# Performance work log

Hardware: AMD Instinct MI355X
Metric: run time of the kernel (lower is better)

Reference implementation:

```python
import jax, jax.numpy as jnp
import numpy as np
from math import sqrt

EMBED_DIM = 1024
PROJ_DIM = 128
BATCH = 4
SEQ = 4096


def setup_inputs() -> dict:
    key = jax.random.key(0)
    ks = jax.random.split(key, 7)
    x = jax.random.normal(ks[0], (BATCH, SEQ, EMBED_DIM), dtype=jnp.float32)
    # nn.Linear default init scale ~ 1/sqrt(fan_in); use small random weights
    s_e = 1.0 / sqrt(EMBED_DIM)
    Wq = jax.random.uniform(ks[1], (EMBED_DIM, PROJ_DIM), jnp.float32, -s_e, s_e)
    bq = jax.random.uniform(ks[2], (PROJ_DIM,), jnp.float32, -s_e, s_e)
    Wk = jax.random.uniform(ks[3], (EMBED_DIM, PROJ_DIM), jnp.float32, -s_e, s_e)
    bk = jax.random.uniform(ks[4], (PROJ_DIM,), jnp.float32, -s_e, s_e)
    Wov = jax.random.uniform(ks[5], (EMBED_DIM, EMBED_DIM), jnp.float32, -s_e, s_e)
    bov = jax.random.uniform(ks[6], (EMBED_DIM,), jnp.float32, -s_e, s_e)
    return {"x": x, "Wq": Wq, "bq": bq, "Wk": Wk, "bk": bk, "Wov": Wov, "bov": bov}


def reference(x, Wq, bq, Wk, bk, Wov, bov):
    # q, k: (b, s, p); ov: (b, s, d)
    queries = jnp.einsum('bse,ep->bsp', x, Wq) + bq
    keys = jnp.einsum('bse,ep->bsp', x, Wk) + bk
    scores = jnp.einsum('bqp,bkp->bqk', queries, keys) / sqrt(PROJ_DIM)
    pattern = jax.nn.softmax(scores, axis=-1)
    ov = jnp.einsum('bse,ed->bsd', x, Wov) + bov
    return jnp.einsum('bqk,bkd->bqd', pattern, ov)
```

## Files before the change

### kernel.cpp

```cpp
#include <hip/hip_runtime.h>
#include <hip/hip_bf16.h>

#define BATCH 4
#define SEQ   4096
#define EMB   1024
#define PDIM  128

using short8   = __attribute__((ext_vector_type(8))) short;
using ushort8  = __attribute__((ext_vector_type(8))) unsigned short;
using ushort4v = __attribute__((ext_vector_type(4))) unsigned short;
using float4v  = __attribute__((ext_vector_type(4))) float;
using float16v = __attribute__((ext_vector_type(16))) float;

__device__ __forceinline__ unsigned short f2bf(float f) {
  union { float f; unsigned int u; } x; x.f = f;
  unsigned int r = x.u + 0x7fffu + ((x.u >> 16) & 1u);
  return (unsigned short)(r >> 16);
}

__device__ __forceinline__ void gld_lds16(const unsigned short* g, unsigned short* l) {
  __builtin_amdgcn_global_load_lds(
      (__attribute__((address_space(1))) void*)(g),
      (__attribute__((address_space(3))) void*)(l), 16, 0, 0);
}

__global__ void xprep_kernel(const float* __restrict__ src,
                             unsigned short* __restrict__ rm,
                             unsigned short* __restrict__ tp) {
  __shared__ float tile[64][65];
  const int tid = threadIdx.x;
  const int z = blockIdx.z;
  const float* s = src + (size_t)z * SEQ * EMB;
  unsigned short* drm = rm + (size_t)z * SEQ * EMB;
  unsigned short* dtp = tp + (size_t)z * SEQ * EMB;
  const int e0 = blockIdx.x * 64, s0 = blockIdx.y * 64;
#pragma unroll
  for (int i = 0; i < 4; i++) {
    int idx = tid + i * 256;
    int sr = idx >> 4, c4 = (idx & 15) * 4;
    float4v v = *(const float4v*)(s + (size_t)(s0 + sr) * EMB + e0 + c4);
    ushort4v o;
    o[0] = f2bf(v[0]); o[1] = f2bf(v[1]); o[2] = f2bf(v[2]); o[3] = f2bf(v[3]);
    *(ushort4v*)(drm + (size_t)(s0 + sr) * EMB + e0 + c4) = o;
    tile[sr][c4] = v[0]; tile[sr][c4 + 1] = v[1];
    tile[sr][c4 + 2] = v[2]; tile[sr][c4 + 3] = v[3];
  }
  __syncthreads();
#pragma unroll
  for (int i = 0; i < 2; i++) {
    int idx = tid + i * 256;
    int e = idx >> 3, sc = idx & 7;
    ushort8 o;
#pragma unroll
    for (int j = 0; j < 8; j++) o[j] = f2bf(tile[sc * 8 + j][e]);
    *(ushort8*)(dtp + (size_t)(e0 + e) * SEQ + s0 + sc * 8) = o;
  }
}

__global__ void wprep_kernel(const float* __restrict__ Wq, const float* __restrict__ Wk,
                             const float* __restrict__ Wov,
                             unsigned short* __restrict__ WqkT, unsigned short* __restrict__ WovT,
                             const float* __restrict__ bq, const float* __restrict__ bk,
                             float* __restrict__ bqk, float* __restrict__ lsum) {
  __shared__ float t[32][33];
  const int bid = blockIdx.x, tid = threadIdx.x;
  const int tx = tid & 31, ty = tid >> 5;
  const float* src; unsigned short* dst; int C, bx, by;
  if (bid < 128)        { src = Wq;  dst = WqkT;                       C = PDIM; int b = bid;        bx = b & 3;  by = b >> 2; }
  else if (bid < 256)   { src = Wk;  dst = WqkT + (size_t)PDIM * EMB;  C = PDIM; int b = bid - 128;  bx = b & 3;  by = b >> 2; }
  else if (bid < 1280)  { src = Wov; dst = WovT;                       C = EMB;  int b = bid - 256;  bx = b & 31; by = b >> 5; }
  else if (bid == 1280) {
    if (tid < 2 * PDIM) bqk[tid] = (tid < PDIM) ? bq[tid] : bk[tid - PDIM];
    return;
  } else {
    lsum[(bid - 1281) * 256 + tid] = 0.f;
    return;
  }
  const int c0 = bx * 32, r0 = by * 32;
#pragma unroll
  for (int i = 0; i < 32; i += 8)
    t[ty + i][tx] = src[(size_t)(r0 + ty + i) * C + c0 + tx];
  __syncthreads();
#pragma unroll
  for (int i = 0; i < 32; i += 8)
    dst[(size_t)(c0 + ty + i) * EMB + r0 + tx] = f2bf(t[tx][ty + i]);
}

template <int NT>
__global__ __launch_bounds__(256, 2) void gemm_kernel(
    const unsigned short* __restrict__ A, int lda, size_t saz,
    const unsigned short* __restrict__ Bt, int ldb, size_t sbz,
    void* __restrict__ Cv, int ldc, size_t scz,
    int K, const float* __restrict__ bias,
    float* __restrict__ lsum, int slz,
    float scale, int mode) {
  constexpr int NTW = NT / 64;
  constexpr int BC  = NT / 32;
  __shared__ __attribute__((aligned(16))) unsigned short As[128 * 64];
  __shared__ __attribute__((aligned(16))) unsigned short Bs[NT * 64];
  const int tid = threadIdx.x;
  const int wave = tid >> 6, lane = tid & 63;
  const int m0 = blockIdx.x * 128, n0 = blockIdx.y * NT;
  const int z = blockIdx.z;
  const int mq = (wave >> 1) * 64, nq = (wave & 1) * (NT / 2);

  A  += (size_t)z * saz;
  Bt += (size_t)z * sbz;

  const int sr = lane >> 3, sc = lane & 7;
  const int kch = (sc ^ sr) * 8;
  const unsigned short* Ag[4]; unsigned short* Al[4];
#pragma unroll
  for (int j = 0; j < 4; j++) {
    int c = wave * 4 + j;
    Ag[j] = A + (size_t)(m0 + c * 8 + sr) * lda + kch;
    Al[j] = As + c * 512;
  }
  const unsigned short* Bg[BC]; unsigned short* Bl[BC];
#pragma unroll
  for (int j = 0; j < BC; j++) {
    int c = wave * BC + j;
    Bg[j] = Bt + (size_t)(n0 + c * 8 + sr) * ldb + kch;
    Bl[j] = Bs + c * 512;
  }

  float16v acc[2][NTW];
#pragma unroll
  for (int i = 0; i < 2; i++)
#pragma unroll
    for (int j = 0; j < NTW; j++)
#pragma unroll
      for (int r = 0; r < 16; r++) acc[i][j][r] = 0.f;

  const int rt = lane & 31;
  const int h  = lane >> 5;
  const int s7 = lane & 7;

  for (int k0 = 0; k0 < K; k0 += 64) {
    if (k0) __syncthreads();
#pragma unroll
    for (int j = 0; j < 4; j++) gld_lds16(Ag[j] + k0, Al[j]);
#pragma unroll
    for (int j = 0; j < BC; j++) gld_lds16(Bg[j] + k0, Bl[j]);
    __syncthreads();
#pragma unroll
    for (int kt = 0; kt < 4; kt++) {
      const int sl = ((kt * 2 + h) ^ s7) * 8;
      short8 af[2], bfr[NTW];
#pragma unroll
      for (int mt = 0; mt < 2; mt++)
        af[mt] = *(const short8*)(As + (mq + mt * 32 + rt) * 64 + sl);
#pragma unroll
      for (int nt = 0; nt < NTW; nt++)
        bfr[nt] = *(const short8*)(Bs + (nq + nt * 32 + rt) * 64 + sl);
#pragma unroll
      for (int mt = 0; mt < 2; mt++)
#pragma unroll
        for (int nt = 0; nt < NTW; nt++)
          acc[mt][nt] = __builtin_amdgcn_mfma_f32_32x32x16_bf16(af[mt], bfr[nt], acc[mt][nt], 0, 0, 0);
    }
  }

  if (mode == 1) {
    unsigned short* Cb = (unsigned short*)Cv + (size_t)z * scz;
    float* ls = lsum + (size_t)z * slz;
#pragma unroll
    for (int mt = 0; mt < 2; mt++) {
      float rs[16];
#pragma unroll
      for (int r = 0; r < 16; r++) rs[r] = 0.f;
#pragma unroll
      for (int r = 0; r < 16; r++) {
        int gm = m0 + mq + mt * 32 + (r & 3) + 8 * (r >> 2) + 4 * h;
#pragma unroll
        for (int nt = 0; nt < NTW; nt++) {
          float e = __expf(acc[mt][nt][r] * scale);
          Cb[(size_t)gm * ldc + n0 + nq + nt * 32 + rt] = f2bf(e);
          rs[r] += e;
        }
      }
#pragma unroll
      for (int r = 0; r < 16; r++) {
        float s = rs[r];
#pragma unroll
        for (int o = 1; o < 32; o <<= 1) s += __shfl_xor(s, o);
        rs[r] = s;
      }
      if (rt == 0)
#pragma unroll
        for (int r = 0; r < 16; r++)
          atomicAdd(&ls[m0 + mq + mt * 32 + (r & 3) + 8 * (r >> 2) + 4 * h], rs[r]);
    }
  } else if (mode == 2) {
    unsigned short* Cb = (unsigned short*)Cv + (size_t)z * scz;
    const float* ls = lsum + (size_t)z * slz;
#pragma unroll
    for (int mt = 0; mt < 2; mt++)
#pragma unroll
      for (int r = 0; r < 16; r++) {
        int gm = m0 + mq + mt * 32 + (r & 3) + 8 * (r >> 2) + 4 * h;
        float li = 1.f / ls[gm];
#pragma unroll
        for (int nt = 0; nt < NTW; nt++)
          Cb[(size_t)gm * ldc + n0 + nq + nt * 32 + rt] = f2bf(acc[mt][nt][r] * li);
      }
  } else {
    float* Cf = (float*)Cv + (size_t)z * scz;
    unsigned short* Cb = (unsigned short*)Cv + (size_t)z * scz;
    float bv[NTW];
#pragma unroll
    for (int nt = 0; nt < NTW; nt++) bv[nt] = bias[n0 + nq + nt * 32 + rt];
#pragma unroll
    for (int mt = 0; mt < 2; mt++)
#pragma unroll
      for (int r = 0; r < 16; r++) {
        int gm = m0 + mq + mt * 32 + (r & 3) + 8 * (r >> 2) + 4 * h;
#pragma unroll
        for (int nt = 0; nt < NTW; nt++) {
          float v = acc[mt][nt][r] + bv[nt];
          if (mode == 0) Cf[(size_t)gm * ldc + n0 + nq + nt * 32 + rt] = v;
          else           Cb[(size_t)gm * ldc + n0 + nq + nt * 32 + rt] = f2bf(v);
        }
      }
  }
}

extern "C" void kernel_launch(void* const* d_in, const int* in_sizes, int n_in,
                              void* d_out, int out_size, void* d_ws, size_t ws_size,
                              hipStream_t stream) {
  const float* x   = (const float*)d_in[0];
  const float* Wq  = (const float*)d_in[1];
  const float* bq  = (const float*)d_in[2];
  const float* Wk  = (const float*)d_in[3];
  const float* bk  = (const float*)d_in[4];
  const float* Wov = (const float*)d_in[5];
  const float* bov = (const float*)d_in[6];
  float* out = (float*)d_out;

  char* ws = (char*)d_ws;
  size_t off = 0;
  auto alloc = [&](size_t bytes) {
    char* p = ws + off;
    off += (bytes + 255) & ~(size_t)255;
    return p;
  };
  const int M = BATCH * SEQ;
  unsigned short* x_bf = (unsigned short*)alloc((size_t)M * EMB * 2);
  unsigned short* xT   = (unsigned short*)alloc((size_t)M * EMB * 2);
  unsigned short* WqkT = (unsigned short*)alloc((size_t)2 * PDIM * EMB * 2);
  unsigned short* WovT = (unsigned short*)alloc((size_t)EMB * EMB * 2);
  float*          bqk  = (float*)alloc(2 * PDIM * sizeof(float));
  unsigned short* qk   = (unsigned short*)alloc((size_t)M * 2 * PDIM * 2);
  float*          linv = (float*)alloc((size_t)M * sizeof(float));
  unsigned short* ctx  = (unsigned short*)alloc((size_t)M * EMB * 2);
  const size_t pslot = (size_t)SEQ * SEQ * 2;
  unsigned short* P = (unsigned short*)(ws + off);
  size_t rem = ws_size > off ? ws_size - off : 0;
  int g = (rem >= 4 * pslot) ? 4 : (rem >= 2 * pslot) ? 2 : 1;

  xprep_kernel<<<dim3(EMB / 64, SEQ / 64, BATCH), 256, 0, stream>>>(x, x_bf, xT);
  wprep_kernel<<<dim3(1345), 256, 0, stream>>>(Wq, Wk, Wov, WqkT, WovT, bq, bk, bqk, linv);

  gemm_kernel<128><<<dim3(M / 128, 2, 1), 256, 0, stream>>>(
      x_bf, EMB, 0, WqkT, EMB, 0, qk, 2 * PDIM, 0, EMB, bqk, nullptr, 0, 1.f, 3);

  const float qscale = 0.08838834764831845f;
  for (int b0 = 0; b0 < BATCH; b0 += g) {
    int gg = (b0 + g <= BATCH) ? g : (BATCH - b0);
    gemm_kernel<256><<<dim3(SEQ / 128, SEQ / 256, gg), 256, 0, stream>>>(
        qk + (size_t)b0 * SEQ * 2 * PDIM, 2 * PDIM, (size_t)SEQ * 2 * PDIM,
        qk + (size_t)b0 * SEQ * 2 * PDIM + PDIM, 2 * PDIM, (size_t)SEQ * 2 * PDIM,
        P, SEQ, (size_t)SEQ * SEQ,
        PDIM, nullptr, linv + (size_t)b0 * SEQ, SEQ, qscale, 1);
    gemm_kernel<256><<<dim3(SEQ / 128, EMB / 256, gg), 256, 0, stream>>>(
        P, SEQ, (size_t)SEQ * SEQ,
        xT + (size_t)b0 * EMB * SEQ, SEQ, (size_t)EMB * SEQ,
        ctx + (size_t)b0 * SEQ * EMB, EMB, (size_t)SEQ * EMB,
        SEQ, nullptr, linv + (size_t)b0 * SEQ, SEQ, 1.f, 2);
  }

  gemm_kernel<256><<<dim3(M / 128, EMB / 256, 1), 256, 0, stream>>>(
      ctx, EMB, 0, WovT, EMB, 0, out, EMB, 0, EMB, bov, nullptr, 0, 1.f, 0);
}
```

Measured before the change: 386.8 us.

## Double-buffer LDS tiles with K=32 stages in GEMM kernel

Splits the K=64 LDS tile into two 32-wide buffers and prefetches the next K-chunk via global_load_lds while computing on the current one, with a new XOR swizzle for the 32-wide row layout. The aim is to overlap global-to-LDS transfer latency with MFMA work instead of load-sync-compute serialization. LDS footprint per block stays the same, but barriers per 64 K double and the wait on the async loads relies on __syncthreads semantics, which risks correctness if vmcnt is not drained.

New measurement: 404.4 us. 1.05x slower.

```diff
diff --git a/kernel.cpp b/kernel.cpp
--- a/kernel.cpp
+++ b/kernel.cpp
@@ -95,9 +95,9 @@
     float* __restrict__ lsum, int slz,
     float scale, int mode) {
   constexpr int NTW = NT / 64;
-  constexpr int BC  = NT / 32;
-  __shared__ __attribute__((aligned(16))) unsigned short As[128 * 64];
-  __shared__ __attribute__((aligned(16))) unsigned short Bs[NT * 64];
+  constexpr int BG  = NT / 64;
+  __shared__ __attribute__((aligned(16))) unsigned short As[2][128 * 32];
+  __shared__ __attribute__((aligned(16))) unsigned short Bs[2][NT * 32];
   const int tid = threadIdx.x;
   const int wave = tid >> 6, lane = tid & 63;
   const int m0 = blockIdx.x * 128, n0 = blockIdx.y * NT;
@@ -107,21 +107,24 @@
   A  += (size_t)z * saz;
   Bt += (size_t)z * sbz;
 
-  const int sr = lane >> 3, sc = lane & 7;
-  const int kch = (sc ^ sr) * 8;
-  const unsigned short* Ag[4]; unsigned short* Al[4];
-#pragma unroll
-  for (int j = 0; j < 4; j++) {
-    int c = wave * 4 + j;
-    Ag[j] = A + (size_t)(m0 + c * 8 + sr) * lda + kch;
-    Al[j] = As + c * 512;
-  }
-  const unsigned short* Bg[BC]; unsigned short* Bl[BC];
-#pragma unroll
-  for (int j = 0; j < BC; j++) {
-    int c = wave * BC + j;
-    Bg[j] = Bt + (size_t)(n0 + c * 8 + sr) * ldb + kch;
-    Bl[j] = Bs + c * 512;
+  const int sr = lane >> 2, sl4 = lane & 3;
+  const unsigned short* Ag[2]; int Ao[2];
+#pragma unroll
+  for (int j = 0; j < 2; j++) {
+    int g = wave * 2 + j;
+    int r = g * 16 + sr;
+    int f = ((r >> 1) & 3) ^ ((r >> 3) & 3);
+    Ag[j] = A + (size_t)(m0 + r) * lda + ((sl4 ^ f) << 3);
+    Ao[j] = g * 512;
+  }
+  const unsigned short* Bg[BG]; int Bo[BG];
+#pragma unroll
+  for (int j = 0; j < BG; j++) {
+    int g = wave * BG + j;
+    int r = g * 16 + sr;
+    int f = ((r >> 1) & 3) ^ ((r >> 3) & 3);
+    Bg[j] = Bt + (size_t)(n0 + r) * ldb + ((sl4 ^ f) << 3);
+    Bo[j] = g * 512;
   }
 
   float16v acc[2][NTW];
@@ -134,31 +137,41 @@
 
   const int rt = lane & 31;
   const int h  = lane >> 5;
-  const int s7 = lane & 7;
-
-  for (int k0 = 0; k0 < K; k0 += 64) {
-    if (k0) __syncthreads();
-#pragma unroll
-    for (int j = 0; j < 4; j++) gld_lds16(Ag[j] + k0, Al[j]);
-#pragma unroll
-    for (int j = 0; j < BC; j++) gld_lds16(Bg[j] + k0, Bl[j]);
-    __syncthreads();
-#pragma unroll
-    for (int kt = 0; kt < 4; kt++) {
-      const int sl = ((kt * 2 + h) ^ s7) * 8;
+  const int fr = ((rt >> 1) & 3) ^ ((rt >> 3) & 3);
+
+  auto stage = [&](int k0, int buf) {
+#pragma unroll
+    for (int j = 0; j < 2; j++) gld_lds16(Ag[j] + k0, &As[buf][Ao[j]]);
+#pragma unroll
+    for (int j = 0; j < BG; j++) gld_lds16(Bg[j] + k0, &Bs[buf][Bo[j]]);
+  };
+  auto compute = [&](int buf) {
+#pragma unroll
+    for (int kt = 0; kt < 2; kt++) {
+      const int sl = (((kt * 2 + h) ^ fr)) << 3;
       short8 af[2], bfr[NTW];
 #pragma unroll
       for (int mt = 0; mt < 2; mt++)
-        af[mt] = *(const short8*)(As + (mq + mt * 32 + rt) * 64 + sl);
+        af[mt] = *(const short8*)(&As[buf][(mq + mt * 32 + rt) * 32 + sl]);
 #pragma unroll
       for (int nt = 0; nt < NTW; nt++)
-        bfr[nt] = *(const short8*)(Bs + (nq + nt * 32 + rt) * 64 + sl);
+        bfr[nt] = *(const short8*)(&Bs[buf][(nq + nt * 32 + rt) * 32 + sl]);
 #pragma unroll
       for (int mt = 0; mt < 2; mt++)
 #pragma unroll
         for (int nt = 0; nt < NTW; nt++)
           acc[mt][nt] = __builtin_amdgcn_mfma_f32_32x32x16_bf16(af[mt], bfr[nt], acc[mt][nt], 0, 0, 0);
     }
+  };
+
+  stage(0, 0);
+  for (int k0 = 0; k0 < K; k0 += 64) {
+    __syncthreads();
+    if (k0 + 32 < K) stage(k0 + 32, 1);
+    compute(0);
+    __syncthreads();
+    if (k0 + 64 < K) stage(k0 + 64, 0);
+    compute(1);
   }
 
   if (mode == 1) {
```
